# Kernel tuning notes

Hardware: AMD Instinct MI355X
Metric: run time of the kernel (lower is better)

## Reference

```python
import jax, jax.numpy as jnp
import numpy as np

T, B, D, H, F, O = 256, 512, 256, 512, 64, 1


def setup_inputs() -> dict:
    key = jax.random.key(0)
    ks = jax.random.split(key, 16)
    s = 0.05
    return {
        "inputs": jax.random.normal(ks[0], (T, B, D), jnp.float32),
        "hidden_init": jnp.zeros((B, H), jnp.float32),
        "cell_init": jnp.zeros((B, H), jnp.float32),
        # LSTMCell params (torch gate order: i, f, g, o)
        "W_ih": jax.random.normal(ks[1], (4 * H, D), jnp.float32) * s,
        "W_hh": jax.random.normal(ks[2], (4 * H, H), jnp.float32) * s,
        "b_ih": jax.random.normal(ks[3], (4 * H,), jnp.float32) * s,
        "b_hh": jax.random.normal(ks[4], (4 * H,), jnp.float32) * s,
        # Attention fc: hidden_dim -> 1
        "attn_w": jax.random.normal(ks[5], (1, H), jnp.float32) * s,
        "attn_b": jax.random.normal(ks[6], (1,), jnp.float32) * s,
        # Output MLP: H->F, F->F, F->F//2, F//2->O
        "W1": jax.random.normal(ks[7], (F, H), jnp.float32) * s,
        "b1": jax.random.normal(ks[8], (F,), jnp.float32) * s,
        "W2": jax.random.normal(ks[9], (F, F), jnp.float32) * s,
        "b2": jax.random.normal(ks[10], (F,), jnp.float32) * s,
        "W3": jax.random.normal(ks[11], (F // 2, F), jnp.float32) * s,
        "b3": jax.random.normal(ks[12], (F // 2,), jnp.float32) * s,
        "W4": jax.random.normal(ks[13], (O, F // 2), jnp.float32) * s,
        "b4": jax.random.normal(ks[14], (O,), jnp.float32) * s,
    }


def _lstm_scan(inputs, h0, c0, W_ih, W_hh, b_ih, b_hh):
    def step(carry, x):
        h, c = carry
        gates = x @ W_ih.T + b_ih + h @ W_hh.T + b_hh  # (B, 4H)
        i, f, g, o = jnp.split(gates, 4, axis=-1)
        c = jax.nn.sigmoid(f) * c + jax.nn.sigmoid(i) * jnp.tanh(g)
        h = jax.nn.sigmoid(o) * jnp.tanh(c)
        return (h, c), h

    (hT, cT), hs = jax.lax.scan(step, (h0, c0), inputs)
    return hT, cT, hs  # hs: (T, B, H)


def reference(inputs, hidden_init, cell_init, W_ih, W_hh, b_ih, b_hh,
              attn_w, attn_b, W1, b1, W2, b2, W3, b3, W4, b4):
    hT, cT, hs = _lstm_scan(inputs, hidden_init, cell_init, W_ih, W_hh, b_ih, b_hh)
    hs = jnp.transpose(hs, (1, 0, 2))            # (B, T, H) == torch.stack(hiddens, dim=1)
    scores = hs @ attn_w.T + attn_b              # (B, T, 1)
    weights = jax.nn.softmax(scores, axis=1)     # softmax over time
    context = jnp.sum(weights * hs, axis=1)      # (B, H)
    x = jnp.tanh(context @ W1.T + b1)
    x = jnp.tanh(x @ W2.T + b2)
    x = jnp.tanh(x @ W3.T + b3)
    out = x @ W4.T + b4                          # (B, O)
    return out, hT, cT
```

## Files before the change

kernel.cpp:

```cpp
#include <hip/hip_runtime.h>


typedef _Float16 f16x8 __attribute__((ext_vector_type(8)));
typedef short    s16x8 __attribute__((ext_vector_type(8)));
typedef float    f32x4 __attribute__((ext_vector_type(4)));

union F16U { f16x8 v; _Float16 e[8]; };

__device__ __forceinline__ float h2f(unsigned short b) {
    return (float)__builtin_bit_cast(_Float16, b);
}
__device__ __forceinline__ unsigned short f2h(float f) {
    return __builtin_bit_cast(unsigned short, (_Float16)f);
}
__device__ __forceinline__ float sigf(float x) { return 1.0f / (1.0f + __expf(-x)); }
__device__ __forceinline__ float tanh_(float x) {
    float e = __expf(-2.0f * fabsf(x));
    float r = (1.0f - e) / (1.0f + e);
    return x < 0.0f ? -r : r;
}
__device__ __forceinline__ unsigned umin_(unsigned a, unsigned b) { return a < b ? a : b; }

__device__ __forceinline__ f16x8 loadA32(const float* p) {
    float4 a = *(const float4*)p, b = *(const float4*)(p + 4);
    F16U r;
    r.e[0]=(_Float16)a.x; r.e[1]=(_Float16)a.y; r.e[2]=(_Float16)a.z; r.e[3]=(_Float16)a.w;
    r.e[4]=(_Float16)b.x; r.e[5]=(_Float16)b.y; r.e[6]=(_Float16)b.z; r.e[7]=(_Float16)b.w;
    return r.v;
}

#define MFMA16(a, b, c) __builtin_amdgcn_mfma_f32_16x16x32_f16((a), (b), (c), 0, 0, 0)
#define BIDX(g, kc) (((g) * 16 + lj) * 96 + ((((kc) * 4) + lq) ^ vg[(g)]))

__device__ __forceinline__ void issue_x(const float* x_t, int arow, int lq, float4* xpf) {
    const float* xb = x_t + (size_t)arow * 256 + lq * 8;
#pragma unroll
    for (int i = 0; i < 8; ++i) {
        asm volatile("global_load_dwordx4 %0, %1, off offset:%c2"
                     : "=v"(xpf[2 * i]) : "v"(xb), "i"(i * 128));
        asm volatile("global_load_dwordx4 %0, %1, off offset:%c2"
                     : "=v"(xpf[2 * i + 1]) : "v"(xb), "i"(i * 128 + 16));
    }
}

__device__ __forceinline__ void gemm_x_reg(const float4* xpf, const f16x8* Wl,
    int lj, int lq, const int* vg,
    f32x4& acc0, f32x4& acc1, f32x4& acc2, f32x4& acc3)
{
    asm volatile("s_waitcnt vmcnt(0)" ::: "memory");
    __builtin_amdgcn_sched_barrier(0);
#pragma unroll
    for (int kc = 0; kc < 8; ++kc) {
        float4 a = xpf[2 * kc], b = xpf[2 * kc + 1];
        F16U r;
        r.e[0]=(_Float16)a.x; r.e[1]=(_Float16)a.y; r.e[2]=(_Float16)a.z; r.e[3]=(_Float16)a.w;
        r.e[4]=(_Float16)b.x; r.e[5]=(_Float16)b.y; r.e[6]=(_Float16)b.z; r.e[7]=(_Float16)b.w;
        acc0 = MFMA16(r.v, Wl[BIDX(0, kc)], acc0);
        acc1 = MFMA16(r.v, Wl[BIDX(1, kc)], acc1);
        acc2 = MFMA16(r.v, Wl[BIDX(2, kc)], acc2);
        acc3 = MFMA16(r.v, Wl[BIDX(3, kc)], acc3);
    }
}

__device__ __forceinline__ void wait_flags(const uint4* fbase, int l, unsigned target) {
    if (l < 32) {
        const uint4* p = fbase + l;
        unsigned m;
        do {
            uint4 v;
            asm volatile("global_load_dwordx4 %0, %1, off sc0 sc1" : "=v"(v) : "v"(p));
            asm volatile("s_waitcnt vmcnt(0)" ::: "memory");
            m = umin_(umin_(v.x, v.y), umin_(v.z, v.w));
        } while (m < target);
    }
    __builtin_amdgcn_sched_barrier(0);
}

__device__ __forceinline__ void gemm_h_ic(const unsigned short* hsrc, const f16x8* Wl,
    int arow, int lj, int lq, const int* vg,
    const unsigned short* ap_dot, const unsigned short* ap_ctx,
    uint4& hdot, uint2& hctx,
    f32x4& acc0, f32x4& acc1, f32x4& acc2, f32x4& acc3)
{
    const unsigned short* hp = hsrc + (size_t)arow * 512 + lq * 8;
    s16x8 hf[16];
#pragma unroll
    for (int i = 0; i < 16; ++i)
        asm volatile("global_load_dwordx4 %0, %1, off offset:%c2 sc0 sc1"
                     : "=v"(hf[i]) : "v"(hp), "i"(i * 64));
    asm volatile("global_load_dwordx4 %0, %1, off sc0 sc1" : "=v"(hdot) : "v"(ap_dot));
    asm volatile("global_load_dwordx2 %0, %1, off sc0 sc1" : "=v"(hctx) : "v"(ap_ctx));

    asm volatile("s_waitcnt vmcnt(10)" ::: "memory");
    __builtin_amdgcn_sched_barrier(0);
#pragma unroll
    for (int kc = 8; kc < 16; ++kc) {
        f16x8 a = __builtin_bit_cast(f16x8, hf[kc - 8]);
        acc0 = MFMA16(a, Wl[BIDX(0, kc)], acc0);
        acc1 = MFMA16(a, Wl[BIDX(1, kc)], acc1);
        acc2 = MFMA16(a, Wl[BIDX(2, kc)], acc2);
        acc3 = MFMA16(a, Wl[BIDX(3, kc)], acc3);
    }
    asm volatile("s_waitcnt vmcnt(2)" ::: "memory");
    __builtin_amdgcn_sched_barrier(0);
#pragma unroll
    for (int kc = 16; kc < 24; ++kc) {
        f16x8 a = __builtin_bit_cast(f16x8, hf[kc - 8]);
        acc0 = MFMA16(a, Wl[BIDX(0, kc)], acc0);
        acc1 = MFMA16(a, Wl[BIDX(1, kc)], acc1);
        acc2 = MFMA16(a, Wl[BIDX(2, kc)], acc2);
        acc3 = MFMA16(a, Wl[BIDX(3, kc)], acc3);
    }
}

__device__ __forceinline__ void gemm_h_init(const float* hsrc, const f16x8* Wl,
    int arow, int lj, int lq, const int* vg,
    f32x4& acc0, f32x4& acc1, f32x4& acc2, f32x4& acc3)
{
    const float* hb = hsrc + (size_t)arow * 512 + lq * 8;
#pragma unroll
    for (int kc = 8; kc < 24; ++kc) {
        f16x8 a = loadA32(hb + (kc - 8) * 32);
        acc0 = MFMA16(a, Wl[BIDX(0, kc)], acc0);
        acc1 = MFMA16(a, Wl[BIDX(1, kc)], acc1);
        acc2 = MFMA16(a, Wl[BIDX(2, kc)], acc2);
        acc3 = MFMA16(a, Wl[BIDX(3, kc)], acc3);
    }
}

__device__ __forceinline__ void attn_apply(uint4 hd, uint2 hc, const float* wv8,
    float s_bias, float& m_r, float& l_r, float ctx[4])
{
    float p = h2f((unsigned short)(hd.x & 0xffffu)) * wv8[0]
            + h2f((unsigned short)(hd.x >> 16))     * wv8[1]
            + h2f((unsigned short)(hd.y & 0xffffu)) * wv8[2]
            + h2f((unsigned short)(hd.y >> 16))     * wv8[3]
            + h2f((unsigned short)(hd.z & 0xffffu)) * wv8[4]
            + h2f((unsigned short)(hd.z >> 16))     * wv8[5]
            + h2f((unsigned short)(hd.w & 0xffffu)) * wv8[6]
            + h2f((unsigned short)(hd.w >> 16))     * wv8[7];
#pragma unroll
    for (int off = 32; off > 0; off >>= 1) p += __shfl_xor(p, off);
    float s = p + s_bias;
    float m_new = fmaxf(m_r, s);
    float scale = __expf(m_r - m_new);
    float pr    = __expf(s - m_new);
    ctx[0] = ctx[0] * scale + pr * h2f((unsigned short)(hc.x & 0xffffu));
    ctx[1] = ctx[1] * scale + pr * h2f((unsigned short)(hc.x >> 16));
    ctx[2] = ctx[2] * scale + pr * h2f((unsigned short)(hc.y & 0xffffu));
    ctx[3] = ctx[3] * scale + pr * h2f((unsigned short)(hc.y >> 16));
    l_r = l_r * scale + pr;
    m_r = m_new;
}

#define SMEM_BYTES 104192

__global__ __launch_bounds__(256, 1) void lstm_persist(
    const float* __restrict__ xg,
    const float* __restrict__ hinit, const float* __restrict__ cinit,
    const float* __restrict__ W_ih, const float* __restrict__ W_hh,
    const float* __restrict__ b_ih, const float* __restrict__ b_hh,
    const float* __restrict__ attn_w, const float* __restrict__ attn_b,
    const float* __restrict__ W1, const float* __restrict__ b1,
    const float* __restrict__ W2, const float* __restrict__ b2,
    const float* __restrict__ W3, const float* __restrict__ b3,
    const float* __restrict__ W4, const float* __restrict__ b4,
    float* __restrict__ out,
    unsigned short* __restrict__ hb0, unsigned short* __restrict__ hb1,
    unsigned* __restrict__ flags)
{
    extern __shared__ char smem[];
    f16x8* Wl    = (f16x8*)smem;
    float* bsum  = (float*)(smem + 98304);
    float* xmlp  = (float*)(smem + 98304 + 512);
    float* x1s   = xmlp + 1024;
    float* x2s   = x1s + 128;
    float* x3s   = x2s + 128;

    const int tid = threadIdx.x, bid = blockIdx.x;
    const int mt = bid & 7, nt = bid >> 3;
    const int hc0 = nt * 16;
    const int w = tid >> 6, l = tid & 63;
    const int lj = l & 15, lq = l >> 4;

    int vg[4];
#pragma unroll
    for (int g = 0; g < 4; ++g) {
        int q = g * 16 + lj;
        vg[g] = ((q >> 3) ^ q) & 7;
    }

    {
        int q = tid >> 2, si = tid & 3;
        int vq = ((q >> 3) ^ q) & 7;
        int grow = (q >> 4) * 512 + hc0 + (q & 15);
        const float* ih = W_ih + (size_t)grow * 256;
        const float* hh = W_hh + (size_t)grow * 512;
        for (int cc = 0; cc < 24; ++cc) {
            int s = si * 24 + cc;
            int k0 = s * 8;
            const float* p = (k0 < 256) ? (ih + k0) : (hh + (k0 - 256));
            float4 a = *(const float4*)p, b = *(const float4*)(p + 4);
            F16U r;
            r.e[0]=(_Float16)a.x; r.e[1]=(_Float16)a.y; r.e[2]=(_Float16)a.z; r.e[3]=(_Float16)a.w;
            r.e[4]=(_Float16)b.x; r.e[5]=(_Float16)b.y; r.e[6]=(_Float16)b.z; r.e[7]=(_Float16)b.w;
            Wl[q * 96 + (s ^ vq)] = r.v;
        }
        if (tid < 64) {
            int gr = (tid >> 4) * 512 + hc0 + (tid & 15);
            bsum[tid] = b_ih[gr] + b_hh[gr];
        }
    }
    __syncthreads();

    const int arow = mt * 64 + w * 16 + lj;
    const int crow = mt * 64 + w * 16 + lq * 4;
    const int ccol = hc0 + lj;
    float creg[4];
#pragma unroll
    for (int r = 0; r < 4; ++r)
        creg[r] = cinit[(size_t)(crow + r) * 512 + ccol];

    float m_r = -__builtin_inff(), l_r = 0.f;
    float ctx[4] = {0.f, 0.f, 0.f, 0.f};
    uint4 hdot = {0, 0, 0, 0}; uint2 hctx = {0, 0};
    const int attr0 = mt * 64 + nt * 2;
    const int arow_at = attr0 + (w >> 1);
    const float s_bias = attn_b[0];
    float wv8[8];
    {
        float4 a = *(const float4*)(attn_w + l * 8);
        float4 b = *(const float4*)(attn_w + l * 8 + 4);
        wv8[0]=a.x; wv8[1]=a.y; wv8[2]=a.z; wv8[3]=a.w;
        wv8[4]=b.x; wv8[5]=b.y; wv8[6]=b.z; wv8[7]=b.w;
    }
    float bs0 = bsum[lj], bs1 = bsum[16 + lj], bs2 = bsum[32 + lj], bs3 = bsum[48 + lj];

    const size_t aoff_dot = (size_t)arow_at * 512 + l * 8;
    const size_t aoff_ctx = (size_t)arow_at * 512 + (w & 1) * 256 + l * 4;
    const uint4* fbase = (const uint4*)flags + mt * 32;
    unsigned* myflag = flags + (size_t)(mt * 32 + nt) * 4 + w;

    float4 xpf[16];
    issue_x(xg, arow, lq, xpf);

    for (int t = 0; t < 256; ++t) {
        unsigned short* hb_cur = (t & 1) ? hb1 : hb0;
        const unsigned short* hb_prev = (t & 1) ? hb0 : hb1;

        f32x4 acc0 = {0,0,0,0}, acc1 = {0,0,0,0}, acc2 = {0,0,0,0}, acc3 = {0,0,0,0};
        gemm_x_reg(xpf, Wl, lj, lq, vg, acc0, acc1, acc2, acc3);

        if (t >= 2) attn_apply(hdot, hctx, wv8, s_bias, m_r, l_r, ctx);

        if (t > 0) {
            wait_flags(fbase, l, (unsigned)t);
            gemm_h_ic(hb_prev, Wl, arow, lj, lq, vg,
                      hb_prev + aoff_dot, hb_prev + aoff_ctx, hdot, hctx,
                      acc0, acc1, acc2, acc3);
        } else {
            gemm_h_init(hinit, Wl, arow, lj, lq, vg, acc0, acc1, acc2, acc3);
        }

#pragma unroll
        for (int r = 0; r < 4; ++r) {
            float ii = sigf(acc0[r] + bs0);
            float ff = sigf(acc1[r] + bs1);
            float gt = tanh_(acc2[r] + bs2);
            float oo = sigf(acc3[r] + bs3);
            float cn = ff * creg[r] + ii * gt;
            creg[r] = cn;
            float hv = oo * tanh_(cn);
            size_t off = (size_t)(crow + r) * 512 + ccol;
            unsigned short hvs = f2h(hv);
            unsigned short* sp = hb_cur + off;
            asm volatile("global_store_short %0, %1, off sc0 sc1"
                         :: "v"(sp), "v"(hvs) : "memory");
            if (t == 255) out[512 + off] = hv;
        }

        const float* xnext = xg + (size_t)(t < 255 ? t + 1 : 255) * 131072;
        issue_x(xnext, arow, lq, xpf);

        asm volatile("s_waitcnt vmcnt(16)" ::: "memory");
        if (l == 0) {
            unsigned fv = (unsigned)(t + 1);
            asm volatile("global_store_dword %0, %1, off sc0 sc1"
                         :: "v"(myflag), "v"(fv) : "memory");
        }
    }

    attn_apply(hdot, hctx, wv8, s_bias, m_r, l_r, ctx);
    wait_flags(fbase, l, 256u);
    {
        const unsigned short* hp = hb1 + aoff_dot;
        const unsigned short* hc = hb1 + aoff_ctx;
        asm volatile("global_load_dwordx4 %0, %1, off sc0 sc1" : "=v"(hdot) : "v"(hp));
        asm volatile("global_load_dwordx2 %0, %1, off sc0 sc1" : "=v"(hctx) : "v"(hc));
        asm volatile("s_waitcnt vmcnt(0)" ::: "memory");
        __builtin_amdgcn_sched_barrier(0);
        attn_apply(hdot, hctx, wv8, s_bias, m_r, l_r, ctx);
    }

#pragma unroll
    for (int r = 0; r < 4; ++r)
        out[512 + 262144 + (size_t)(crow + r) * 512 + ccol] = creg[r];

    {
        float linv = 1.0f / l_r;
        int row = tid >> 7, coff = (tid & 127) * 4;
#pragma unroll
        for (int i = 0; i < 4; ++i) xmlp[row * 512 + coff + i] = ctx[i] * linv;
    }
    __syncthreads();
    if (tid < 128) {
        int r = tid >> 6, f = tid & 63;
        const float* wp = W1 + (size_t)f * 512;
        const float* xp = xmlp + r * 512;
        float a = b1[f];
        for (int j = 0; j < 512; ++j) a = fmaf(xp[j], wp[j], a);
        x1s[r * 64 + f] = tanh_(a);
    }
    __syncthreads();
    if (tid < 128) {
        int r = tid >> 6, f = tid & 63;
        const float* wp = W2 + f * 64;
        const float* xp = x1s + r * 64;
        float a = b2[f];
        for (int j = 0; j < 64; ++j) a = fmaf(xp[j], wp[j], a);
        x2s[r * 64 + f] = tanh_(a);
    }
    __syncthreads();
    if (tid < 64) {
        int r = tid >> 5, f = tid & 31;
        const float* wp = W3 + f * 64;
        const float* xp = x2s + r * 64;
        float a = b3[f];
        for (int j = 0; j < 64; ++j) a = fmaf(xp[j], wp[j], a);
        x3s[r * 32 + f] = tanh_(a);
    }
    __syncthreads();
    if (tid < 2) {
        const float* xp = x3s + tid * 32;
        float a = b4[0];
        for (int j = 0; j < 32; ++j) a = fmaf(xp[j], W4[j], a);
        out[attr0 + tid] = a;
    }
}

extern "C" void kernel_launch(void* const* d_in, const int* in_sizes, int n_in,
                              void* d_out, int out_size, void* d_ws, size_t ws_size,
                              hipStream_t stream) {
    const float* xg     = (const float*)d_in[0];
    const float* hinit  = (const float*)d_in[1];
    const float* cinit  = (const float*)d_in[2];
    const float* W_ih   = (const float*)d_in[3];
    const float* W_hh   = (const float*)d_in[4];
    const float* b_ih   = (const float*)d_in[5];
    const float* b_hh   = (const float*)d_in[6];
    const float* attn_w = (const float*)d_in[7];
    const float* attn_b = (const float*)d_in[8];
    const float* W1 = (const float*)d_in[9],  *b1 = (const float*)d_in[10];
    const float* W2 = (const float*)d_in[11], *b2 = (const float*)d_in[12];
    const float* W3 = (const float*)d_in[13], *b3 = (const float*)d_in[14];
    const float* W4 = (const float*)d_in[15], *b4 = (const float*)d_in[16];

    unsigned short* hb0 = (unsigned short*)d_ws;
    unsigned short* hb1 = hb0 + 262144;
    unsigned* flags = (unsigned*)((char*)d_ws + 1048576);

    hipMemsetAsync(flags, 0, 4096, stream);
    hipFuncSetAttribute((const void*)lstm_persist,
                        hipFuncAttributeMaxDynamicSharedMemorySize, SMEM_BYTES);
    lstm_persist<<<256, 256, SMEM_BYTES, stream>>>(
        xg, hinit, cinit, W_ih, W_hh, b_ih, b_hh, attn_w, attn_b,
        W1, b1, W2, b2, W3, b3, W4, b4,
        (float*)d_out, hb0, hb1, flags);
}
```

Baseline: 1.698 ms.

## Write full hidden-state history so recurrent loads can use cached access

When the workspace is large enough, each timestep's fp16 hidden state goes to its own slice of a full T×B×H history buffer instead of a ping-pong pair. Because no address is ever rewritten, the per-step loads of h_prev and the attention operands can drop the sc0/sc1 system-coherent bits and use normal cached loads, cutting latency on the serial recurrence. The cost is a workspace of about 128 MB and more write traffic. Correctness relies on no stale cache lines existing for addresses that have never been read before. The old ping-pong kernel is kept as a fallback.

```diff
diff --git a/kernel.cpp b/kernel.cpp
--- a/kernel.cpp
+++ b/kernel.cpp
@@ -76,7 +76,8 @@
     __builtin_amdgcn_sched_barrier(0);
 }
 
-__device__ __forceinline__ void gemm_h_ic(const unsigned short* hsrc, const f16x8* Wl,
+template<bool SC>
+__device__ __forceinline__ void gemm_h(const unsigned short* hsrc, const f16x8* Wl,
     int arow, int lj, int lq, const int* vg,
     const unsigned short* ap_dot, const unsigned short* ap_ctx,
     uint4& hdot, uint2& hctx,
@@ -85,11 +86,21 @@
     const unsigned short* hp = hsrc + (size_t)arow * 512 + lq * 8;
     s16x8 hf[16];
 #pragma unroll
-    for (int i = 0; i < 16; ++i)
-        asm volatile("global_load_dwordx4 %0, %1, off offset:%c2 sc0 sc1"
-                     : "=v"(hf[i]) : "v"(hp), "i"(i * 64));
-    asm volatile("global_load_dwordx4 %0, %1, off sc0 sc1" : "=v"(hdot) : "v"(ap_dot));
-    asm volatile("global_load_dwordx2 %0, %1, off sc0 sc1" : "=v"(hctx) : "v"(ap_ctx));
+    for (int i = 0; i < 16; ++i) {
+        if constexpr (SC)
+            asm volatile("global_load_dwordx4 %0, %1, off offset:%c2 sc0 sc1"
+                         : "=v"(hf[i]) : "v"(hp), "i"(i * 64));
+        else
+            asm volatile("global_load_dwordx4 %0, %1, off offset:%c2"
+                         : "=v"(hf[i]) : "v"(hp), "i"(i * 64));
+    }
+    if constexpr (SC) {
+        asm volatile("global_load_dwordx4 %0, %1, off sc0 sc1" : "=v"(hdot) : "v"(ap_dot));
+        asm volatile("global_load_dwordx2 %0, %1, off sc0 sc1" : "=v"(hctx) : "v"(ap_ctx));
+    } else {
+        asm volatile("global_load_dwordx4 %0, %1, off" : "=v"(hdot) : "v"(ap_dot));
+        asm volatile("global_load_dwordx2 %0, %1, off" : "=v"(hctx) : "v"(ap_ctx));
+    }
 
     asm volatile("s_waitcnt vmcnt(10)" ::: "memory");
     __builtin_amdgcn_sched_barrier(0);
@@ -155,7 +166,8 @@
 
 #define SMEM_BYTES 104192
 
-__global__ __launch_bounds__(256, 1) void lstm_persist(
+template<bool HIST>
+__device__ __forceinline__ void lstm_body(
     const float* __restrict__ xg,
     const float* __restrict__ hinit, const float* __restrict__ cinit,
     const float* __restrict__ W_ih, const float* __restrict__ W_hh,
@@ -166,7 +178,7 @@
     const float* __restrict__ W3, const float* __restrict__ b3,
     const float* __restrict__ W4, const float* __restrict__ b4,
     float* __restrict__ out,
-    unsigned short* __restrict__ hb0, unsigned short* __restrict__ hb1,
+    unsigned short* __restrict__ hbA, unsigned short* __restrict__ hbB,
     unsigned* __restrict__ flags)
 {
     extern __shared__ char smem[];
@@ -245,8 +257,15 @@
     issue_x(xg, arow, lq, xpf);
 
     for (int t = 0; t < 256; ++t) {
-        unsigned short* hb_cur = (t & 1) ? hb1 : hb0;
-        const unsigned short* hb_prev = (t & 1) ? hb0 : hb1;
+        unsigned short* hb_cur;
+        const unsigned short* hb_prev;
+        if constexpr (HIST) {
+            hb_cur  = hbA + (size_t)t * 262144;
+            hb_prev = hb_cur - 262144;
+        } else {
+            hb_cur  = (t & 1) ? hbB : hbA;
+            hb_prev = (t & 1) ? hbA : hbB;
+        }
 
         f32x4 acc0 = {0,0,0,0}, acc1 = {0,0,0,0}, acc2 = {0,0,0,0}, acc3 = {0,0,0,0};
         gemm_x_reg(xpf, Wl, lj, lq, vg, acc0, acc1, acc2, acc3);
@@ -255,9 +274,9 @@
 
         if (t > 0) {
             wait_flags(fbase, l, (unsigned)t);
-            gemm_h_ic(hb_prev, Wl, arow, lj, lq, vg,
-                      hb_prev + aoff_dot, hb_prev + aoff_ctx, hdot, hctx,
-                      acc0, acc1, acc2, acc3);
+            gemm_h<!HIST>(hb_prev, Wl, arow, lj, lq, vg,
+                          hb_prev + aoff_dot, hb_prev + aoff_ctx, hdot, hctx,
+                          acc0, acc1, acc2, acc3);
         } else {
             gemm_h_init(hinit, Wl, arow, lj, lq, vg, acc0, acc1, acc2, acc3);
         }
@@ -293,10 +312,16 @@
     attn_apply(hdot, hctx, wv8, s_bias, m_r, l_r, ctx);
     wait_flags(fbase, l, 256u);
     {
-        const unsigned short* hp = hb1 + aoff_dot;
-        const unsigned short* hc = hb1 + aoff_ctx;
-        asm volatile("global_load_dwordx4 %0, %1, off sc0 sc1" : "=v"(hdot) : "v"(hp));
-        asm volatile("global_load_dwordx2 %0, %1, off sc0 sc1" : "=v"(hctx) : "v"(hc));
+        const unsigned short* hlast = HIST ? (hbA + (size_t)255 * 262144) : hbB;
+        const unsigned short* hp = hlast + aoff_dot;
+        const unsigned short* hc = hlast + aoff_ctx;
+        if constexpr (HIST) {
+            asm volatile("global_load_dwordx4 %0, %1, off" : "=v"(hdot) : "v"(hp));
+            asm volatile("global_load_dwordx2 %0, %1, off" : "=v"(hctx) : "v"(hc));
+        } else {
+            asm volatile("global_load_dwordx4 %0, %1, off sc0 sc1" : "=v"(hdot) : "v"(hp));
+            asm volatile("global_load_dwordx2 %0, %1, off sc0 sc1" : "=v"(hctx) : "v"(hc));
+        }
         asm volatile("s_waitcnt vmcnt(0)" ::: "memory");
         __builtin_amdgcn_sched_barrier(0);
         attn_apply(hdot, hctx, wv8, s_bias, m_r, l_r, ctx);
@@ -346,6 +371,41 @@
         for (int j = 0; j < 32; ++j) a = fmaf(xp[j], W4[j], a);
         out[attr0 + tid] = a;
     }
+}
+
+__global__ __launch_bounds__(256, 1) void lstm_hist(
+    const float* __restrict__ xg,
+    const float* __restrict__ hinit, const float* __restrict__ cinit,
+    const float* __restrict__ W_ih, const float* __restrict__ W_hh,
+    const float* __restrict__ b_ih, const float* __restrict__ b_hh,
+    const float* __restrict__ attn_w, const float* __restrict__ attn_b,
+    const float* __restrict__ W1, const float* __restrict__ b1,
+    const float* __restrict__ W2, const float* __restrict__ b2,
+    const float* __restrict__ W3, const float* __restrict__ b3,
+    const float* __restrict__ W4, const float* __restrict__ b4,
+    float* __restrict__ out,
+    unsigned short* __restrict__ hs, unsigned* __restrict__ flags)
+{
+    lstm_body<true>(xg, hinit, cinit, W_ih, W_hh, b_ih, b_hh, attn_w, attn_b,
+                    W1, b1, W2, b2, W3, b3, W4, b4, out, hs, nullptr, flags);
+}
+
+__global__ __launch_bounds__(256, 1) void lstm_legacy(
+    const float* __restrict__ xg,
+    const float* __restrict__ hinit, const float* __restrict__ cinit,
+    const float* __restrict__ W_ih, const float* __restrict__ W_hh,
+    const float* __restrict__ b_ih, const float* __restrict__ b_hh,
+    const float* __restrict__ attn_w, const float* __restrict__ attn_b,
+    const float* __restrict__ W1, const float* __restrict__ b1,
+    const float* __restrict__ W2, const float* __restrict__ b2,
+    const float* __restrict__ W3, const float* __restrict__ b3,
+    const float* __restrict__ W4, const float* __restrict__ b4,
+    float* __restrict__ out,
+    unsigned short* __restrict__ hb0, unsigned short* __restrict__ hb1,
+    unsigned* __restrict__ flags)
+{
+    lstm_body<false>(xg, hinit, cinit, W_ih, W_hh, b_ih, b_hh, attn_w, attn_b,
+                     W1, b1, W2, b2, W3, b3, W4, b4, out, hb0, hb1, flags);
 }
 
 extern "C" void kernel_launch(void* const* d_in, const int* in_sizes, int n_in,
@@ -365,15 +425,27 @@
     const float* W3 = (const float*)d_in[13], *b3 = (const float*)d_in[14];
     const float* W4 = (const float*)d_in[15], *b4 = (const float*)d_in[16];
 
-    unsigned short* hb0 = (unsigned short*)d_ws;
-    unsigned short* hb1 = hb0 + 262144;
-    unsigned* flags = (unsigned*)((char*)d_ws + 1048576);
-
-    hipMemsetAsync(flags, 0, 4096, stream);
-    hipFuncSetAttribute((const void*)lstm_persist,
-                        hipFuncAttributeMaxDynamicSharedMemorySize, SMEM_BYTES);
-    lstm_persist<<<256, 256, SMEM_BYTES, stream>>>(
-        xg, hinit, cinit, W_ih, W_hh, b_ih, b_hh, attn_w, attn_b,
-        W1, b1, W2, b2, W3, b3, W4, b4,
-        (float*)d_out, hb0, hb1, flags);
-}
+    const size_t HS_BYTES = (size_t)256 * 512 * 512 * 2;
+    if (ws_size >= HS_BYTES + 4096) {
+        unsigned short* hs = (unsigned short*)d_ws;
+        unsigned* flags = (unsigned*)((char*)d_ws + HS_BYTES);
+        hipMemsetAsync(flags, 0, 4096, stream);
+        hipFuncSetAttribute((const void*)lstm_hist,
+                            hipFuncAttributeMaxDynamicSharedMemorySize, SMEM_BYTES);
+        lstm_hist<<<256, 256, SMEM_BYTES, stream>>>(
+            xg, hinit, cinit, W_ih, W_hh, b_ih, b_hh, attn_w, attn_b,
+            W1, b1, W2, b2, W3, b3, W4, b4,
+            (float*)d_out, hs, flags);
+    } else {
+        unsigned short* hb0 = (unsigned short*)d_ws;
+        unsigned short* hb1 = hb0 + 262144;
+        unsigned* flags = (unsigned*)((char*)d_ws + 1048576);
+        hipMemsetAsync(flags, 0, 4096, stream);
+        hipFuncSetAttribute((const void*)lstm_legacy,
+                            hipFuncAttributeMaxDynamicSharedMemorySize, SMEM_BYTES);
+        lstm_legacy<<<256, 256, SMEM_BYTES, stream>>>(
+            xg, hinit, cinit, W_ih, W_hh, b_ih, b_hh, attn_w, attn_b,
+            W1, b1, W2, b2, W3, b3, W4, b4,
+            (float*)d_out, hb0, hb1, flags);
+    }
+}
```

Result: no change. 1.668 ms (-1.7%).

## Hoist input projection into a precompute phase and keep full hidden history

Applied to the files above, without the earlier changes.

Adds a two-phase persistent kernel. The first phase computes x·W_ihᵀ for all timesteps with MFMA and writes it as fp16 to a large workspace buffer, then a grid-wide atomic barrier starts the recurrence. The recurrent loop now only does the h·W_hhᵀ GEMM, seeded from prefetched precomputed gate values, which shortens the serial per-step critical path and shrinks the LDS weight footprint. Hidden states go to a per-timestep history buffer instead of a ping-pong pair, so h reads can drop the cache-bypass bits. The cost is writing and reading about 512 MB of gate data, fp16 rounding of the input projection, and a fallback kernel path when the workspace is too small.

```diff
diff --git a/kernel.cpp b/kernel.cpp
--- a/kernel.cpp
+++ b/kernel.cpp
@@ -6,6 +6,7 @@
 typedef float    f32x4 __attribute__((ext_vector_type(4)));
 
 union F16U { f16x8 v; _Float16 e[8]; };
+union U2F16 { uint2 u; _Float16 e[4]; };
 
 __device__ __forceinline__ float h2f(unsigned short b) {
     return (float)__builtin_bit_cast(_Float16, b);
@@ -30,7 +31,8 @@
 }
 
 #define MFMA16(a, b, c) __builtin_amdgcn_mfma_f32_16x16x32_f16((a), (b), (c), 0, 0, 0)
-#define BIDX(g, kc) (((g) * 16 + lj) * 96 + ((((kc) * 4) + lq) ^ vg[(g)]))
+#define BIDX(g, kc)  (((g) * 16 + lj) * 96 + ((((kc) * 4) + lq) ^ vg[(g)]))
+#define BIDX2(g, kc) (((g) * 16 + lj) * 64 + (((((kc) - 8) * 4) + lq) ^ vg[(g)]))
 
 __device__ __forceinline__ void issue_x(const float* x_t, int arow, int lq, float4* xpf) {
     const float* xb = x_t + (size_t)arow * 256 + lq * 8;
@@ -76,7 +78,7 @@
     __builtin_amdgcn_sched_barrier(0);
 }
 
-__device__ __forceinline__ void gemm_h_ic(const unsigned short* hsrc, const f16x8* Wl,
+__device__ __forceinline__ void gemm_h_fb(const unsigned short* hsrc, const f16x8* Wl,
     int arow, int lj, int lq, const int* vg,
     const unsigned short* ap_dot, const unsigned short* ap_ctx,
     uint4& hdot, uint2& hctx,
@@ -86,10 +88,10 @@
     s16x8 hf[16];
 #pragma unroll
     for (int i = 0; i < 16; ++i)
-        asm volatile("global_load_dwordx4 %0, %1, off offset:%c2 sc0 sc1"
+        asm volatile("global_load_dwordx4 %0, %1, off offset:%c2"
                      : "=v"(hf[i]) : "v"(hp), "i"(i * 64));
-    asm volatile("global_load_dwordx4 %0, %1, off sc0 sc1" : "=v"(hdot) : "v"(ap_dot));
-    asm volatile("global_load_dwordx2 %0, %1, off sc0 sc1" : "=v"(hctx) : "v"(ap_ctx));
+    asm volatile("global_load_dwordx4 %0, %1, off" : "=v"(hdot) : "v"(ap_dot));
+    asm volatile("global_load_dwordx2 %0, %1, off" : "=v"(hctx) : "v"(ap_ctx));
 
     asm volatile("s_waitcnt vmcnt(10)" ::: "memory");
     __builtin_amdgcn_sched_barrier(0);
@@ -113,7 +115,7 @@
     }
 }
 
-__device__ __forceinline__ void gemm_h_init(const float* hsrc, const f16x8* Wl,
+__device__ __forceinline__ void gemm_h_init_fb(const float* hsrc, const f16x8* Wl,
     int arow, int lj, int lq, const int* vg,
     f32x4& acc0, f32x4& acc1, f32x4& acc2, f32x4& acc3)
 {
@@ -125,6 +127,58 @@
         acc1 = MFMA16(a, Wl[BIDX(1, kc)], acc1);
         acc2 = MFMA16(a, Wl[BIDX(2, kc)], acc2);
         acc3 = MFMA16(a, Wl[BIDX(3, kc)], acc3);
+    }
+}
+
+__device__ __forceinline__ void gemm_h2(const unsigned short* hsrc, const f16x8* Wl,
+    int arow, int lj, int lq, const int* vg,
+    const unsigned short* ap_dot, const unsigned short* ap_ctx,
+    uint4& hdot, uint2& hctx,
+    f32x4& acc0, f32x4& acc1, f32x4& acc2, f32x4& acc3)
+{
+    const unsigned short* hp = hsrc + (size_t)arow * 512 + lq * 8;
+    s16x8 hf[16];
+#pragma unroll
+    for (int i = 0; i < 16; ++i)
+        asm volatile("global_load_dwordx4 %0, %1, off offset:%c2"
+                     : "=v"(hf[i]) : "v"(hp), "i"(i * 64));
+    asm volatile("global_load_dwordx4 %0, %1, off" : "=v"(hdot) : "v"(ap_dot));
+    asm volatile("global_load_dwordx2 %0, %1, off" : "=v"(hctx) : "v"(ap_ctx));
+
+    asm volatile("s_waitcnt vmcnt(10)" ::: "memory");
+    __builtin_amdgcn_sched_barrier(0);
+#pragma unroll
+    for (int kc = 8; kc < 16; ++kc) {
+        f16x8 a = __builtin_bit_cast(f16x8, hf[kc - 8]);
+        acc0 = MFMA16(a, Wl[BIDX2(0, kc)], acc0);
+        acc1 = MFMA16(a, Wl[BIDX2(1, kc)], acc1);
+        acc2 = MFMA16(a, Wl[BIDX2(2, kc)], acc2);
+        acc3 = MFMA16(a, Wl[BIDX2(3, kc)], acc3);
+    }
+    asm volatile("s_waitcnt vmcnt(2)" ::: "memory");
+    __builtin_amdgcn_sched_barrier(0);
+#pragma unroll
+    for (int kc = 16; kc < 24; ++kc) {
+        f16x8 a = __builtin_bit_cast(f16x8, hf[kc - 8]);
+        acc0 = MFMA16(a, Wl[BIDX2(0, kc)], acc0);
+        acc1 = MFMA16(a, Wl[BIDX2(1, kc)], acc1);
+        acc2 = MFMA16(a, Wl[BIDX2(2, kc)], acc2);
+        acc3 = MFMA16(a, Wl[BIDX2(3, kc)], acc3);
+    }
+}
+
+__device__ __forceinline__ void gemm_h_init2(const float* hsrc, const f16x8* Wl,
+    int arow, int lj, int lq, const int* vg,
+    f32x4& acc0, f32x4& acc1, f32x4& acc2, f32x4& acc3)
+{
+    const float* hb = hsrc + (size_t)arow * 512 + lq * 8;
+#pragma unroll
+    for (int kc = 8; kc < 24; ++kc) {
+        f16x8 a = loadA32(hb + (kc - 8) * 32);
+        acc0 = MFMA16(a, Wl[BIDX2(0, kc)], acc0);
+        acc1 = MFMA16(a, Wl[BIDX2(1, kc)], acc1);
+        acc2 = MFMA16(a, Wl[BIDX2(2, kc)], acc2);
+        acc3 = MFMA16(a, Wl[BIDX2(3, kc)], acc3);
     }
 }
 
@@ -153,9 +207,10 @@
     m_r = m_new;
 }
 
-#define SMEM_BYTES 104192
-
-__global__ __launch_bounds__(256, 1) void lstm_persist(
+#define SMEM_FB  104192
+#define SMEM_2PH 131072
+
+__global__ __launch_bounds__(256, 1) void lstm_2ph(
     const float* __restrict__ xg,
     const float* __restrict__ hinit, const float* __restrict__ cinit,
     const float* __restrict__ W_ih, const float* __restrict__ W_hh,
@@ -166,22 +221,107 @@
     const float* __restrict__ W3, const float* __restrict__ b3,
     const float* __restrict__ W4, const float* __restrict__ b4,
     float* __restrict__ out,
-    unsigned short* __restrict__ hb0, unsigned short* __restrict__ hb1,
-    unsigned* __restrict__ flags)
+    unsigned short* __restrict__ gxs, unsigned short* __restrict__ hs,
+    unsigned* __restrict__ flags, unsigned* __restrict__ bar)
 {
     extern __shared__ char smem[];
+    const int tid = threadIdx.x, bid = blockIdx.x;
+    const int w = tid >> 6, l = tid & 63;
+    const int lj = l & 15, lq = l >> 4;
+
+    {
+        f16x8* Wp = (f16x8*)smem;
+        const int tg = bid >> 3, cg = bid & 7;
+        {
+            int row = tid;
+            int vq = ((row >> 3) ^ row) & 7;
+            const float* p0 = W_ih + ((size_t)(cg * 256 + row)) * 256;
+            for (int s = 0; s < 32; ++s)
+                Wp[row * 32 + (s ^ vq)] = loadA32(p0 + s * 8);
+        }
+        __syncthreads();
+
+        float4 xpf[16];
+        f16x8 A0[8], A1[8];
+        for (int tl = 0; tl < 8; ++tl) {
+            int tt = tg * 8 + tl;
+            const float* xt = xg + (size_t)tt * 131072;
+            for (int rtp = 0; rtp < 4; ++rtp) {
+                int brow0 = w * 128 + rtp * 32;
+                issue_x(xt, brow0 + lj, lq, xpf);
+                asm volatile("s_waitcnt vmcnt(0)" ::: "memory");
+                __builtin_amdgcn_sched_barrier(0);
+#pragma unroll
+                for (int kc = 0; kc < 8; ++kc) {
+                    float4 a = xpf[2*kc], b = xpf[2*kc+1];
+                    F16U r;
+                    r.e[0]=(_Float16)a.x; r.e[1]=(_Float16)a.y; r.e[2]=(_Float16)a.z; r.e[3]=(_Float16)a.w;
+                    r.e[4]=(_Float16)b.x; r.e[5]=(_Float16)b.y; r.e[6]=(_Float16)b.z; r.e[7]=(_Float16)b.w;
+                    A0[kc] = r.v;
+                }
+                issue_x(xt, brow0 + 16 + lj, lq, xpf);
+                asm volatile("s_waitcnt vmcnt(0)" ::: "memory");
+                __builtin_amdgcn_sched_barrier(0);
+#pragma unroll
+                for (int kc = 0; kc < 8; ++kc) {
+                    float4 a = xpf[2*kc], b = xpf[2*kc+1];
+                    F16U r;
+                    r.e[0]=(_Float16)a.x; r.e[1]=(_Float16)a.y; r.e[2]=(_Float16)a.z; r.e[3]=(_Float16)a.w;
+                    r.e[4]=(_Float16)b.x; r.e[5]=(_Float16)b.y; r.e[6]=(_Float16)b.z; r.e[7]=(_Float16)b.w;
+                    A1[kc] = r.v;
+                }
+#pragma unroll
+                for (int ct = 0; ct < 16; ++ct) {
+                    int row2 = ct * 16 + lj;
+                    int vgc = ((row2 >> 3) ^ row2) & 7;
+                    f32x4 a0 = {0,0,0,0}, a1 = {0,0,0,0};
+#pragma unroll
+                    for (int kc = 0; kc < 8; ++kc) {
+                        f16x8 Bf = Wp[row2 * 32 + ((kc * 4 + lq) ^ vgc)];
+                        a0 = MFMA16(A0[kc], Bf, a0);
+                        a1 = MFMA16(A1[kc], Bf, a1);
+                    }
+                    size_t base = ((size_t)tt * 2048 + (size_t)(cg * 256 + ct * 16 + lj)) * 512
+                                  + brow0 + lq * 4;
+                    U2F16 s0, s1;
+                    s0.e[0]=(_Float16)a0[0]; s0.e[1]=(_Float16)a0[1];
+                    s0.e[2]=(_Float16)a0[2]; s0.e[3]=(_Float16)a0[3];
+                    s1.e[0]=(_Float16)a1[0]; s1.e[1]=(_Float16)a1[1];
+                    s1.e[2]=(_Float16)a1[2]; s1.e[3]=(_Float16)a1[3];
+                    unsigned short* sp0 = gxs + base;
+                    unsigned short* sp1 = gxs + base + 16;
+                    asm volatile("global_store_dwordx2 %0, %1, off sc0 sc1"
+                                 :: "v"(sp0), "v"(s0.u) : "memory");
+                    asm volatile("global_store_dwordx2 %0, %1, off sc0 sc1"
+                                 :: "v"(sp1), "v"(s1.u) : "memory");
+                }
+            }
+        }
+    }
+
+    asm volatile("s_waitcnt vmcnt(0)" ::: "memory");
+    __syncthreads();
+    if (tid == 0) {
+        __threadfence();
+        atomicAdd((int*)bar, 1);
+        unsigned a;
+        const unsigned* bp = bar;
+        do {
+            asm volatile("global_load_dword %0, %1, off sc0 sc1" : "=v"(a) : "v"(bp));
+            asm volatile("s_waitcnt vmcnt(0)" ::: "memory");
+        } while (a < 256u);
+    }
+    __syncthreads();
+
     f16x8* Wl    = (f16x8*)smem;
-    float* bsum  = (float*)(smem + 98304);
-    float* xmlp  = (float*)(smem + 98304 + 512);
+    float* bsum  = (float*)(smem + 65536);
+    float* xmlp  = (float*)(smem + 66048);
     float* x1s   = xmlp + 1024;
     float* x2s   = x1s + 128;
     float* x3s   = x2s + 128;
 
-    const int tid = threadIdx.x, bid = blockIdx.x;
     const int mt = bid & 7, nt = bid >> 3;
     const int hc0 = nt * 16;
-    const int w = tid >> 6, l = tid & 63;
-    const int lj = l & 15, lq = l >> 4;
 
     int vg[4];
 #pragma unroll
@@ -194,17 +334,10 @@
         int q = tid >> 2, si = tid & 3;
         int vq = ((q >> 3) ^ q) & 7;
         int grow = (q >> 4) * 512 + hc0 + (q & 15);
-        const float* ih = W_ih + (size_t)grow * 256;
         const float* hh = W_hh + (size_t)grow * 512;
-        for (int cc = 0; cc < 24; ++cc) {
-            int s = si * 24 + cc;
-            int k0 = s * 8;
-            const float* p = (k0 < 256) ? (ih + k0) : (hh + (k0 - 256));
-            float4 a = *(const float4*)p, b = *(const float4*)(p + 4);
-            F16U r;
-            r.e[0]=(_Float16)a.x; r.e[1]=(_Float16)a.y; r.e[2]=(_Float16)a.z; r.e[3]=(_Float16)a.w;
-            r.e[4]=(_Float16)b.x; r.e[5]=(_Float16)b.y; r.e[6]=(_Float16)b.z; r.e[7]=(_Float16)b.w;
-            Wl[q * 96 + (s ^ vq)] = r.v;
+        for (int cc = 0; cc < 16; ++cc) {
+            int s = si * 16 + cc;
+            Wl[q * 64 + (s ^ vq)] = loadA32(hh + s * 8);
         }
         if (tid < 64) {
             int gr = (tid >> 4) * 512 + hc0 + (tid & 15);
@@ -241,25 +374,48 @@
     const uint4* fbase = (const uint4*)flags + mt * 32;
     unsigned* myflag = flags + (size_t)(mt * 32 + nt) * 4 + w;
 
-    float4 xpf[16];
-    issue_x(xg, arow, lq, xpf);
+    const size_t gxbase = ((size_t)nt * 16 + lj) * 512 + mt * 64 + w * 16 + lq * 4;
+    uint2 gxr[4];
+#pragma unroll
+    for (int g = 0; g < 4; ++g) {
+        const unsigned short* p = gxs + (size_t)g * 262144 + gxbase;
+        asm volatile("global_load_dwordx2 %0, %1, off sc0 sc1" : "=v"(gxr[g]) : "v"(p));
+    }
 
     for (int t = 0; t < 256; ++t) {
-        unsigned short* hb_cur = (t & 1) ? hb1 : hb0;
-        const unsigned short* hb_prev = (t & 1) ? hb0 : hb1;
-
-        f32x4 acc0 = {0,0,0,0}, acc1 = {0,0,0,0}, acc2 = {0,0,0,0}, acc3 = {0,0,0,0};
-        gemm_x_reg(xpf, Wl, lj, lq, vg, acc0, acc1, acc2, acc3);
+        unsigned short* hb_cur = hs + (size_t)t * 262144;
+        const unsigned short* hb_prev = hb_cur - 262144;
+
+        asm volatile("s_waitcnt vmcnt(0)" ::: "memory");
+        __builtin_amdgcn_sched_barrier(0);
+        f32x4 acc0, acc1, acc2, acc3;
+        acc0[0]=h2f((unsigned short)(gxr[0].x & 0xffffu)); acc0[1]=h2f((unsigned short)(gxr[0].x >> 16));
+        acc0[2]=h2f((unsigned short)(gxr[0].y & 0xffffu)); acc0[3]=h2f((unsigned short)(gxr[0].y >> 16));
+        acc1[0]=h2f((unsigned short)(gxr[1].x & 0xffffu)); acc1[1]=h2f((unsigned short)(gxr[1].x >> 16));
+        acc1[2]=h2f((unsigned short)(gxr[1].y & 0xffffu)); acc1[3]=h2f((unsigned short)(gxr[1].y >> 16));
+        acc2[0]=h2f((unsigned short)(gxr[2].x & 0xffffu)); acc2[1]=h2f((unsigned short)(gxr[2].x >> 16));
+        acc2[2]=h2f((unsigned short)(gxr[2].y & 0xffffu)); acc2[3]=h2f((unsigned short)(gxr[2].y >> 16));
+        acc3[0]=h2f((unsigned short)(gxr[3].x & 0xffffu)); acc3[1]=h2f((unsigned short)(gxr[3].x >> 16));
+        acc3[2]=h2f((unsigned short)(gxr[3].y & 0xffffu)); acc3[3]=h2f((unsigned short)(gxr[3].y >> 16));
+
+        {
+            int tn = (t < 255) ? (t + 1) : 255;
+#pragma unroll
+            for (int g = 0; g < 4; ++g) {
+                const unsigned short* p = gxs + (size_t)tn * 1048576 + (size_t)g * 262144 + gxbase;
+                asm volatile("global_load_dwordx2 %0, %1, off sc0 sc1" : "=v"(gxr[g]) : "v"(p));
+            }
+        }
 
         if (t >= 2) attn_apply(hdot, hctx, wv8, s_bias, m_r, l_r, ctx);
 
         if (t > 0) {
             wait_flags(fbase, l, (unsigned)t);
-            gemm_h_ic(hb_prev, Wl, arow, lj, lq, vg,
-                      hb_prev + aoff_dot, hb_prev + aoff_ctx, hdot, hctx,
-                      acc0, acc1, acc2, acc3);
+            gemm_h2(hb_prev, Wl, arow, lj, lq, vg,
+                    hb_prev + aoff_dot, hb_prev + aoff_ctx, hdot, hctx,
+                    acc0, acc1, acc2, acc3);
         } else {
-            gemm_h_init(hinit, Wl, arow, lj, lq, vg, acc0, acc1, acc2, acc3);
+            gemm_h_init2(hinit, Wl, arow, lj, lq, vg, acc0, acc1, acc2, acc3);
         }
 
 #pragma unroll
@@ -279,6 +435,192 @@
             if (t == 255) out[512 + off] = hv;
         }
 
+        asm volatile("s_waitcnt vmcnt(0)" ::: "memory");
+        if (l == 0) {
+            unsigned fv = (unsigned)(t + 1);
+            asm volatile("global_store_dword %0, %1, off sc0 sc1"
+                         :: "v"(myflag), "v"(fv) : "memory");
+        }
+    }
+
+    attn_apply(hdot, hctx, wv8, s_bias, m_r, l_r, ctx);
+    wait_flags(fbase, l, 256u);
+    {
+        const unsigned short* hlast = hs + (size_t)255 * 262144;
+        const unsigned short* hp = hlast + aoff_dot;
+        const unsigned short* hc = hlast + aoff_ctx;
+        asm volatile("global_load_dwordx4 %0, %1, off" : "=v"(hdot) : "v"(hp));
+        asm volatile("global_load_dwordx2 %0, %1, off" : "=v"(hctx) : "v"(hc));
+        asm volatile("s_waitcnt vmcnt(0)" ::: "memory");
+        __builtin_amdgcn_sched_barrier(0);
+        attn_apply(hdot, hctx, wv8, s_bias, m_r, l_r, ctx);
+    }
+
+#pragma unroll
+    for (int r = 0; r < 4; ++r)
+        out[512 + 262144 + (size_t)(crow + r) * 512 + ccol] = creg[r];
+
+    {
+        float linv = 1.0f / l_r;
+        int row = tid >> 7, coff = (tid & 127) * 4;
+#pragma unroll
+        for (int i = 0; i < 4; ++i) xmlp[row * 512 + coff + i] = ctx[i] * linv;
+    }
+    __syncthreads();
+    if (tid < 128) {
+        int r = tid >> 6, f = tid & 63;
+        const float* wp = W1 + (size_t)f * 512;
+        const float* xp = xmlp + r * 512;
+        float a = b1[f];
+        for (int j = 0; j < 512; ++j) a = fmaf(xp[j], wp[j], a);
+        x1s[r * 64 + f] = tanh_(a);
+    }
+    __syncthreads();
+    if (tid < 128) {
+        int r = tid >> 6, f = tid & 63;
+        const float* wp = W2 + f * 64;
+        const float* xp = x1s + r * 64;
+        float a = b2[f];
+        for (int j = 0; j < 64; ++j) a = fmaf(xp[j], wp[j], a);
+        x2s[r * 64 + f] = tanh_(a);
+    }
+    __syncthreads();
+    if (tid < 64) {
+        int r = tid >> 5, f = tid & 31;
+        const float* wp = W3 + f * 64;
+        const float* xp = x2s + r * 64;
+        float a = b3[f];
+        for (int j = 0; j < 64; ++j) a = fmaf(xp[j], wp[j], a);
+        x3s[r * 32 + f] = tanh_(a);
+    }
+    __syncthreads();
+    if (tid < 2) {
+        const float* xp = x3s + tid * 32;
+        float a = b4[0];
+        for (int j = 0; j < 32; ++j) a = fmaf(xp[j], W4[j], a);
+        out[attr0 + tid] = a;
+    }
+}
+
+__global__ __launch_bounds__(256, 1) void lstm_hist(
+    const float* __restrict__ xg,
+    const float* __restrict__ hinit, const float* __restrict__ cinit,
+    const float* __restrict__ W_ih, const float* __restrict__ W_hh,
+    const float* __restrict__ b_ih, const float* __restrict__ b_hh,
+    const float* __restrict__ attn_w, const float* __restrict__ attn_b,
+    const float* __restrict__ W1, const float* __restrict__ b1,
+    const float* __restrict__ W2, const float* __restrict__ b2,
+    const float* __restrict__ W3, const float* __restrict__ b3,
+    const float* __restrict__ W4, const float* __restrict__ b4,
+    float* __restrict__ out,
+    unsigned short* __restrict__ hbA, unsigned* __restrict__ flags)
+{
+    extern __shared__ char smem[];
+    f16x8* Wl    = (f16x8*)smem;
+    float* bsum  = (float*)(smem + 98304);
+    float* xmlp  = (float*)(smem + 98304 + 512);
+    float* x1s   = xmlp + 1024;
+    float* x2s   = x1s + 128;
+    float* x3s   = x2s + 128;
+
+    const int tid = threadIdx.x, bid = blockIdx.x;
+    const int mt = bid & 7, nt = bid >> 3;
+    const int hc0 = nt * 16;
+    const int w = tid >> 6, l = tid & 63;
+    const int lj = l & 15, lq = l >> 4;
+
+    int vg[4];
+#pragma unroll
+    for (int g = 0; g < 4; ++g) {
+        int q = g * 16 + lj;
+        vg[g] = ((q >> 3) ^ q) & 7;
+    }
+
+    {
+        int q = tid >> 2, si = tid & 3;
+        int vq = ((q >> 3) ^ q) & 7;
+        int grow = (q >> 4) * 512 + hc0 + (q & 15);
+        const float* ih = W_ih + (size_t)grow * 256;
+        const float* hh = W_hh + (size_t)grow * 512;
+        for (int cc = 0; cc < 24; ++cc) {
+            int s = si * 24 + cc;
+            int k0 = s * 8;
+            const float* p = (k0 < 256) ? (ih + k0) : (hh + (k0 - 256));
+            Wl[q * 96 + (s ^ vq)] = loadA32(p);
+        }
+        if (tid < 64) {
+            int gr = (tid >> 4) * 512 + hc0 + (tid & 15);
+            bsum[tid] = b_ih[gr] + b_hh[gr];
+        }
+    }
+    __syncthreads();
+
+    const int arow = mt * 64 + w * 16 + lj;
+    const int crow = mt * 64 + w * 16 + lq * 4;
+    const int ccol = hc0 + lj;
+    float creg[4];
+#pragma unroll
+    for (int r = 0; r < 4; ++r)
+        creg[r] = cinit[(size_t)(crow + r) * 512 + ccol];
+
+    float m_r = -__builtin_inff(), l_r = 0.f;
+    float ctx[4] = {0.f, 0.f, 0.f, 0.f};
+    uint4 hdot = {0, 0, 0, 0}; uint2 hctx = {0, 0};
+    const int attr0 = mt * 64 + nt * 2;
+    const int arow_at = attr0 + (w >> 1);
+    const float s_bias = attn_b[0];
+    float wv8[8];
+    {
+        float4 a = *(const float4*)(attn_w + l * 8);
+        float4 b = *(const float4*)(attn_w + l * 8 + 4);
+        wv8[0]=a.x; wv8[1]=a.y; wv8[2]=a.z; wv8[3]=a.w;
+        wv8[4]=b.x; wv8[5]=b.y; wv8[6]=b.z; wv8[7]=b.w;
+    }
+    float bs0 = bsum[lj], bs1 = bsum[16 + lj], bs2 = bsum[32 + lj], bs3 = bsum[48 + lj];
+
+    const size_t aoff_dot = (size_t)arow_at * 512 + l * 8;
+    const size_t aoff_ctx = (size_t)arow_at * 512 + (w & 1) * 256 + l * 4;
+    const uint4* fbase = (const uint4*)flags + mt * 32;
+    unsigned* myflag = flags + (size_t)(mt * 32 + nt) * 4 + w;
+
+    float4 xpf[16];
+    issue_x(xg, arow, lq, xpf);
+
+    for (int t = 0; t < 256; ++t) {
+        unsigned short* hb_cur = hbA + (size_t)t * 262144;
+        const unsigned short* hb_prev = hb_cur - 262144;
+
+        f32x4 acc0 = {0,0,0,0}, acc1 = {0,0,0,0}, acc2 = {0,0,0,0}, acc3 = {0,0,0,0};
+        gemm_x_reg(xpf, Wl, lj, lq, vg, acc0, acc1, acc2, acc3);
+
+        if (t >= 2) attn_apply(hdot, hctx, wv8, s_bias, m_r, l_r, ctx);
+
+        if (t > 0) {
+            wait_flags(fbase, l, (unsigned)t);
+            gemm_h_fb(hb_prev, Wl, arow, lj, lq, vg,
+                      hb_prev + aoff_dot, hb_prev + aoff_ctx, hdot, hctx,
+                      acc0, acc1, acc2, acc3);
+        } else {
+            gemm_h_init_fb(hinit, Wl, arow, lj, lq, vg, acc0, acc1, acc2, acc3);
+        }
+
+#pragma unroll
+        for (int r = 0; r < 4; ++r) {
+            float ii = sigf(acc0[r] + bs0);
+            float ff = sigf(acc1[r] + bs1);
+            float gt = tanh_(acc2[r] + bs2);
+            float oo = sigf(acc3[r] + bs3);
+            float cn = ff * creg[r] + ii * gt;
+            creg[r] = cn;
+            float hv = oo * tanh_(cn);
+            size_t off = (size_t)(crow + r) * 512 + ccol;
+            unsigned short hvs = f2h(hv);
+            unsigned short* sp = hb_cur + off;
+            asm volatile("global_store_short %0, %1, off sc0 sc1"
+                         :: "v"(sp), "v"(hvs) : "memory");
+            if (t == 255) out[512 + off] = hv;
+        }
+
         const float* xnext = xg + (size_t)(t < 255 ? t + 1 : 255) * 131072;
         issue_x(xnext, arow, lq, xpf);
 
@@ -293,10 +635,11 @@
     attn_apply(hdot, hctx, wv8, s_bias, m_r, l_r, ctx);
     wait_flags(fbase, l, 256u);
     {
-        const unsigned short* hp = hb1 + aoff_dot;
-        const unsigned short* hc = hb1 + aoff_ctx;
-        asm volatile("global_load_dwordx4 %0, %1, off sc0 sc1" : "=v"(hdot) : "v"(hp));
-        asm volatile("global_load_dwordx2 %0, %1, off sc0 sc1" : "=v"(hctx) : "v"(hc));
+        const unsigned short* hlast = hbA + (size_t)255 * 262144;
+        const unsigned short* hp = hlast + aoff_dot;
+        const unsigned short* hc = hlast + aoff_ctx;
+        asm volatile("global_load_dwordx4 %0, %1, off" : "=v"(hdot) : "v"(hp));
+        asm volatile("global_load_dwordx2 %0, %1, off" : "=v"(hctx) : "v"(hc));
         asm volatile("s_waitcnt vmcnt(0)" ::: "memory");
         __builtin_amdgcn_sched_barrier(0);
         attn_apply(hdot, hctx, wv8, s_bias, m_r, l_r, ctx);
@@ -365,15 +708,30 @@
     const float* W3 = (const float*)d_in[13], *b3 = (const float*)d_in[14];
     const float* W4 = (const float*)d_in[15], *b4 = (const float*)d_in[16];
 
-    unsigned short* hb0 = (unsigned short*)d_ws;
-    unsigned short* hb1 = hb0 + 262144;
-    unsigned* flags = (unsigned*)((char*)d_ws + 1048576);
-
-    hipMemsetAsync(flags, 0, 4096, stream);
-    hipFuncSetAttribute((const void*)lstm_persist,
-                        hipFuncAttributeMaxDynamicSharedMemorySize, SMEM_BYTES);
-    lstm_persist<<<256, 256, SMEM_BYTES, stream>>>(
-        xg, hinit, cinit, W_ih, W_hh, b_ih, b_hh, attn_w, attn_b,
-        W1, b1, W2, b2, W3, b3, W4, b4,
-        (float*)d_out, hb0, hb1, flags);
-}
+    const size_t GX_BYTES = 536870912ull;
+    const size_t HS_BYTES = 134217728ull;
+
+    if (ws_size >= GX_BYTES + HS_BYTES + 8192) {
+        unsigned short* gxs = (unsigned short*)d_ws;
+        unsigned short* hs  = (unsigned short*)((char*)d_ws + GX_BYTES);
+        unsigned* flags = (unsigned*)((char*)d_ws + GX_BYTES + HS_BYTES);
+        unsigned* bar   = (unsigned*)((char*)d_ws + GX_BYTES + HS_BYTES + 4096);
+        hipMemsetAsync(flags, 0, 8192, stream);
+        hipFuncSetAttribute((const void*)lstm_2ph,
+                            hipFuncAttributeMaxDynamicSharedMemorySize, SMEM_2PH);
+        lstm_2ph<<<256, 256, SMEM_2PH, stream>>>(
+            xg, hinit, cinit, W_ih, W_hh, b_ih, b_hh, attn_w, attn_b,
+            W1, b1, W2, b2, W3, b3, W4, b4,
+            (float*)d_out, gxs, hs, flags, bar);
+    } else {
+        unsigned short* hs = (unsigned short*)d_ws;
+        unsigned* flags = (unsigned*)((char*)d_ws + HS_BYTES);
+        hipMemsetAsync(flags, 0, 4096, stream);
+        hipFuncSetAttribute((const void*)lstm_hist,
+                            hipFuncAttributeMaxDynamicSharedMemorySize, SMEM_FB);
+        lstm_hist<<<256, 256, SMEM_FB, stream>>>(
+            xg, hinit, cinit, W_ih, W_hh, b_ih, b_hh, attn_w, attn_b,
+            W1, b1, W2, b2, W3, b3, W4, b4,
+            (float*)d_out, hs, flags);
+    }
+}
```

Result: faster. 1.609 ms (-5.2%).
